# Performance work log

Measured on AMD Instinct MI355X. Metric: run time of the kernel, lower is better.

Reference implementation:

```python
import jax, jax.numpy as jnp
import numpy as np
from jax.scipy.special import logsumexp

NUM_TAGS = 48
SEQ_LEN = 512
BATCH = 1024


def setup_inputs() -> dict:
    key = jax.random.key(0)
    k_em, k_tags, k_tr, k_st, k_en = jax.random.split(key, 5)
    emissions = jax.random.normal(k_em, (SEQ_LEN, BATCH, NUM_TAGS), dtype=jnp.float32)
    tags = jax.random.randint(k_tags, (SEQ_LEN, BATCH), 0, NUM_TAGS, dtype=jnp.int64)
    mask = jnp.ones((SEQ_LEN, BATCH), dtype=jnp.int32)
    # CRF parameters, uniform(-0.1, 0.1) like reset_parameters
    transitions = jax.random.uniform(k_tr, (NUM_TAGS, NUM_TAGS), jnp.float32, -0.1, 0.1)
    start_transitions = jax.random.uniform(k_st, (NUM_TAGS,), jnp.float32, -0.1, 0.1)
    end_transitions = jax.random.uniform(k_en, (NUM_TAGS,), jnp.float32, -0.1, 0.1)
    return {
        "emissions": emissions,
        "tags": tags,
        "mask": mask,
        "transitions": transitions,
        "start_transitions": start_transitions,
        "end_transitions": end_transitions,
    }


def _score(emissions, tags, mask, transitions, start_transitions, end_transitions):
    # emissions: (S,B,T)  tags/mask: (S,B)
    S, B = tags.shape
    batch_idx = jnp.arange(B)
    maskf = mask.astype(emissions.dtype)
    # emission score at the gold tag for every timestep: (S,B)
    em_sc = jnp.take_along_axis(emissions, tags[..., None], axis=2)[..., 0]
    score = start_transitions[tags[0]] + em_sc[0]
    # transition score for steps 1..S-1: (S-1,B)
    trans_sc = transitions[tags[:-1], tags[1:]]
    score = score + ((trans_sc + em_sc[1:]) * maskf[1:]).sum(axis=0)
    valid_last_idx = mask.astype(jnp.int32).sum(axis=0) - 1  # (B,)
    last_tags = tags[valid_last_idx, batch_idx]
    return score + end_transitions[last_tags]


def _partition(emissions, mask, transitions, start_transitions, end_transitions):
    alpha0 = start_transitions[None, :] + emissions[0]  # (B,T)

    def step(alpha, inp):
        em_i, m_i = inp  # (B,T), (B,)
        # (B,T_prev,1) + (T_prev,T_cur) + (B,1,T_cur) -> logsumexp over prev
        cur = logsumexp(alpha[:, :, None] + transitions[None, :, :] + em_i[:, None, :], axis=1)
        alpha = jnp.where(m_i.astype(bool)[:, None], cur, alpha)
        return alpha, None

    alpha, _ = jax.lax.scan(step, alpha0, (emissions[1:], mask[1:]))
    return logsumexp(alpha + end_transitions[None, :], axis=1)  # (B,)


def reference(emissions, tags, mask, transitions, start_transitions, end_transitions):
    score = _score(emissions, tags, mask, transitions, start_transitions, end_transitions)
    partition = _partition(emissions, mask, transitions, start_transitions, end_transitions)
    nllh = partition - score
    return nllh.sum()  # reduction='sum'
```

## Files before the change

### kernel.cpp

```cpp
#include <hip/hip_runtime.h>

#define S 512
#define B 1024
#define K 48
#define LN2 0.6931471805599453f
#define PF 8

__global__ void __launch_bounds__(64) zero_out(float* o) {
    if (threadIdx.x == 0) o[0] = 0.f;
}

__device__ __forceinline__ float matvec48(const float4* f, const float* eT) {
    float s0 = 0.f, s1 = 0.f, s2 = 0.f, s3 = 0.f;
    #pragma unroll
    for (int i = 0; i < 12; ++i) {
        s0 = fmaf(f[i].x, eT[4 * i + 0], s0);
        s1 = fmaf(f[i].y, eT[4 * i + 1], s1);
        s2 = fmaf(f[i].z, eT[4 * i + 2], s2);
        s3 = fmaf(f[i].w, eT[4 * i + 3], s3);
    }
    return (s0 + s1) + (s2 + s3);
}

__global__ void __launch_bounds__(64) crf_kernel(
    const float* __restrict__ em, const int* __restrict__ tags,
    const int* __restrict__ mask, const float* __restrict__ trans,
    const float* __restrict__ start_tr, const float* __restrict__ end_tr,
    float* __restrict__ out)
{
    const int b    = blockIdx.x;
    const int lane = threadIdx.x;
    __shared__ __align__(16) float sh[K];

    float sc = 0.f;
    int mcnt = 0;
    #pragma unroll
    for (int i = 0; i < S / 64; ++i) {
        int t   = lane + 64 * i;
        int tag = tags[t * B + b];
        int mk  = mask[t * B + b];
        mcnt += mk;
        if (t == 0) {
            sc += start_tr[tag] + em[(size_t)b * K + tag];
        } else {
            int tagp  = tags[(t - 1) * B + b];
            float add = trans[tagp * K + tag] + em[((size_t)t * B + b) * K + tag];
            sc += mk ? add : 0.f;
        }
    }
    #pragma unroll
    for (int off = 32; off > 0; off >>= 1) {
        sc   += __shfl_xor(sc, off);
        mcnt += __shfl_xor(mcnt, off);
    }
    int last_t = mcnt - 1;
    if (last_t < 0) last_t += S;
    sc += end_tr[tags[last_t * B + b]];

    const int  j      = (lane < K) ? lane : 0;
    const bool active = lane < K;

    float eT[K];
    #pragma unroll
    for (int k = 0; k < K; ++k)
        eT[k] = __expf(trans[k * K + j]);

    float a      = __expf(start_tr[j] + em[(size_t)b * K + j]);
    int   offset = 0;
    float scale  = 1.0f;

    if (active) sh[j] = a;
    const float4* shv = (const float4*)sh;
    float4 f[12];
    #pragma unroll
    for (int i = 0; i < 12; ++i) f[i] = shv[i];

    float em_raw[PF];
    int   mk_n[PF];
    #pragma unroll
    for (int i = 0; i < PF; ++i) {
        em_raw[i] = em[((size_t)(1 + i) * B + b) * K + j];
        mk_n[i]   = mask[(size_t)(1 + i) * B + b];
    }
    float eexp_cur = __expf(em_raw[0]);

#define STEP(u_, t_, PFON_)                                                     \
    do {                                                                        \
        float s_   = matvec48(f, eT);                                           \
        float an_  = s_ * eexp_cur;                                             \
        a = mk_n[u_] ? an_ : a;                       \
        a *= scale;                          \
        if (lane < K) sh[lane] = a;                                             \
        _Pragma("unroll")                                                       \
        for (int i2_ = 0; i2_ < 12; ++i2_) f[i2_] = shv[i2_];                   \
        eexp_cur = __expf(em_raw[((u_) + 1) & 7]);           \
        if (PFON_) {                                                            \
            int tp_ = (t_) + PF;                                                \
            if (tp_ < S) {                                                      \
                em_raw[u_] = em[((size_t)tp_ * B + b) * K + j];                 \
                mk_n[u_]   = mask[(size_t)tp_ * B + b];                         \
            }                                                                   \
        }                                                                       \
        if (((u_) & 3) == 3) {               \
            int bits_ = __builtin_amdgcn_readlane(__float_as_int(a), 0);        \
            int E_    = ((bits_ >> 23) & 255) - 127;                            \
            offset += E_;                                                       \
            scale = __int_as_float((127 - E_) << 23);                           \
        } else {                                                                \
            scale = 1.0f;                                                       \
        }                                                                       \
    } while (0)

    for (int t0 = 1; t0 <= S - 2 * PF + 1; t0 += PF) {
        #pragma unroll
        for (int u = 0; u < PF; ++u) {
            STEP(u, t0 + u, true);
        }
    }
    #pragma unroll
    for (int u = 0; u < PF - 1; ++u) {
        STEP(u, (S - PF + 1) + u, false);
    }
#undef STEP

    float val = active ? a * __expf(end_tr[j]) : 0.f;
    #pragma unroll
    for (int off = 32; off > 0; off >>= 1) val += __shfl_xor(val, off);
    float partition = (float)offset * LN2 + __logf(val);

    if (lane == 0) atomicAdd(out, partition - sc);
}

extern "C" void kernel_launch(void* const* d_in, const int* in_sizes, int n_in,
                              void* d_out, int out_size, void* d_ws, size_t ws_size,
                              hipStream_t stream) {
    const float* em       = (const float*)d_in[0];
    const int*   tags     = (const int*)d_in[1];
    const int*   mask     = (const int*)d_in[2];
    const float* trans    = (const float*)d_in[3];
    const float* start_tr = (const float*)d_in[4];
    const float* end_tr   = (const float*)d_in[5];
    float* out = (float*)d_out;

    zero_out<<<dim3(1), dim3(64), 0, stream>>>(out);
    crf_kernel<<<dim3(B), dim3(64), 0, stream>>>(em, tags, mask, trans,
                                                 start_tr, end_tr, out);
}
```

Measured before the change: 319.4 us.

## Process two batch rows per wavefront to interleave independent recurrences

```diff
diff --git a/kernel.cpp b/kernel.cpp
--- a/kernel.cpp
+++ b/kernel.cpp
@@ -5,6 +5,7 @@
 #define K 48
 #define LN2 0.6931471805599453f
 #define PF 8
+#define NBLK 512
 
 __global__ void __launch_bounds__(64) zero_out(float* o) {
     if (threadIdx.x == 0) o[0] = 0.f;
@@ -28,107 +29,131 @@
     const float* __restrict__ start_tr, const float* __restrict__ end_tr,
     float* __restrict__ out)
 {
-    const int b    = blockIdx.x;
     const int lane = threadIdx.x;
-    __shared__ __align__(16) float sh[K];
+    const int b0   = blockIdx.x;
+    const int b1   = blockIdx.x + NBLK;
+    __shared__ __align__(16) float sh[2][K];
 
-    float sc = 0.f;
-    int mcnt = 0;
+    float scA = 0.f, scB = 0.f;
+    int mcA = 0, mcB = 0;
     #pragma unroll
     for (int i = 0; i < S / 64; ++i) {
-        int t   = lane + 64 * i;
-        int tag = tags[t * B + b];
-        int mk  = mask[t * B + b];
-        mcnt += mk;
-        if (t == 0) {
-            sc += start_tr[tag] + em[(size_t)b * K + tag];
-        } else {
-            int tagp  = tags[(t - 1) * B + b];
-            float add = trans[tagp * K + tag] + em[((size_t)t * B + b) * K + tag];
-            sc += mk ? add : 0.f;
+        int t = lane + 64 * i;
+        {
+            int tag = tags[t * B + b0];
+            int mk  = mask[t * B + b0];
+            mcA += mk;
+            if (t == 0) scA += start_tr[tag] + em[(size_t)b0 * K + tag];
+            else {
+                int tagp = tags[(t - 1) * B + b0];
+                float add = trans[tagp * K + tag] + em[((size_t)t * B + b0) * K + tag];
+                scA += mk ? add : 0.f;
+            }
+        }
+        {
+            int tag = tags[t * B + b1];
+            int mk  = mask[t * B + b1];
+            mcB += mk;
+            if (t == 0) scB += start_tr[tag] + em[(size_t)b1 * K + tag];
+            else {
+                int tagp = tags[(t - 1) * B + b1];
+                float add = trans[tagp * K + tag] + em[((size_t)t * B + b1) * K + tag];
+                scB += mk ? add : 0.f;
+            }
         }
     }
     #pragma unroll
     for (int off = 32; off > 0; off >>= 1) {
-        sc   += __shfl_xor(sc, off);
-        mcnt += __shfl_xor(mcnt, off);
+        scA += __shfl_xor(scA, off);
+        scB += __shfl_xor(scB, off);
+        mcA += __shfl_xor(mcA, off);
+        mcB += __shfl_xor(mcB, off);
     }
-    int last_t = mcnt - 1;
-    if (last_t < 0) last_t += S;
-    sc += end_tr[tags[last_t * B + b]];
+    int lA = mcA - 1; if (lA < 0) lA += S;
+    int lB = mcB - 1; if (lB < 0) lB += S;
+    scA += end_tr[tags[lA * B + b0]];
+    scB += end_tr[tags[lB * B + b1]];
 
     const int  j      = (lane < K) ? lane : 0;
     const bool active = lane < K;
 
     float eT[K];
     #pragma unroll
-    for (int k = 0; k < K; ++k)
-        eT[k] = __expf(trans[k * K + j]);
+    for (int k = 0; k < K; ++k) eT[k] = __expf(trans[k * K + j]);
 
-    float a      = __expf(start_tr[j] + em[(size_t)b * K + j]);
-    int   offset = 0;
-    float scale  = 1.0f;
+    float aA = __expf(start_tr[j] + em[(size_t)b0 * K + j]);
+    float aB = __expf(start_tr[j] + em[(size_t)b1 * K + j]);
+    int   offA = 0, offB = 0;
+    float sclA = 1.f, sclB = 1.f;
 
-    if (active) sh[j] = a;
-    const float4* shv = (const float4*)sh;
-    float4 f[12];
-    #pragma unroll
-    for (int i = 0; i < 12; ++i) f[i] = shv[i];
+    if (active) { sh[0][j] = aA; sh[1][j] = aB; }
+    const float4* shA = (const float4*)sh[0];
+    const float4* shB = (const float4*)sh[1];
 
-    float em_raw[PF];
-    int   mk_n[PF];
+    float emA[PF], emB[PF];
+    int   mkA[PF], mkB[PF];
     #pragma unroll
     for (int i = 0; i < PF; ++i) {
-        em_raw[i] = em[((size_t)(1 + i) * B + b) * K + j];
-        mk_n[i]   = mask[(size_t)(1 + i) * B + b];
+        emA[i] = em[((size_t)(1 + i) * B + b0) * K + j];
+        emB[i] = em[((size_t)(1 + i) * B + b1) * K + j];
+        mkA[i] = mask[(size_t)(1 + i) * B + b0];
+        mkB[i] = mask[(size_t)(1 + i) * B + b1];
     }
-    float eexp_cur = __expf(em_raw[0]);
+    float eexpA = __expf(emA[0]);
+    float eexpB = __expf(emB[0]);
 
-#define STEP(u_, t_, PFON_)                                                     \
+#define STEP2(u_, t_, PFON_)                                                    \
     do {                                                                        \
-        float s_   = matvec48(f, eT);                                           \
-        float an_  = s_ * eexp_cur;                                             \
-        a = mk_n[u_] ? an_ : a;                       \
-        a *= scale;                          \
-        if (lane < K) sh[lane] = a;                                             \
-        _Pragma("unroll")                                                       \
-        for (int i2_ = 0; i2_ < 12; ++i2_) f[i2_] = shv[i2_];                   \
-        eexp_cur = __expf(em_raw[((u_) + 1) & 7]);           \
+        float4 fA_[12], fB_[12];                                                \
+        _Pragma("unroll") for (int i_ = 0; i_ < 12; ++i_) fA_[i_] = shA[i_];    \
+        _Pragma("unroll") for (int i_ = 0; i_ < 12; ++i_) fB_[i_] = shB[i_];    \
+        float sA_ = matvec48(fA_, eT);                                          \
+        float sB_ = matvec48(fB_, eT);                                          \
+        float anA_ = sA_ * eexpA;                                               \
+        float anB_ = sB_ * eexpB;                                               \
+        aA = mkA[u_] ? anA_ : aA;  aA *= sclA;                                  \
+        aB = mkB[u_] ? anB_ : aB;  aB *= sclB;                                  \
+        if (lane < K) { sh[0][lane] = aA; sh[1][lane] = aB; }                   \
+        eexpA = __expf(emA[((u_) + 1) & 7]);                                    \
+        eexpB = __expf(emB[((u_) + 1) & 7]);                                    \
         if (PFON_) {                                                            \
             int tp_ = (t_) + PF;                                                \
             if (tp_ < S) {                                                      \
-                em_raw[u_] = em[((size_t)tp_ * B + b) * K + j];                 \
-                mk_n[u_]   = mask[(size_t)tp_ * B + b];                         \
+                emA[u_] = em[((size_t)tp_ * B + b0) * K + j];                   \
+                emB[u_] = em[((size_t)tp_ * B + b1) * K + j];                   \
+                mkA[u_] = mask[(size_t)tp_ * B + b0];                           \
+                mkB[u_] = mask[(size_t)tp_ * B + b1];                           \
             }                                                                   \
         }                                                                       \
-        if (((u_) & 3) == 3) {               \
-            int bits_ = __builtin_amdgcn_readlane(__float_as_int(a), 0);        \
-            int E_    = ((bits_ >> 23) & 255) - 127;                            \
-            offset += E_;                                                       \
-            scale = __int_as_float((127 - E_) << 23);                           \
-        } else {                                                                \
-            scale = 1.0f;                                                       \
-        }                                                                       \
+        if (((u_) & 7) == 7) {      \
+            int bA_ = __builtin_amdgcn_readlane(__float_as_int(aA), 0);         \
+            int bB_ = __builtin_amdgcn_readlane(__float_as_int(aB), 0);         \
+            int EA_ = ((bA_ >> 23) & 255) - 127;                                \
+            int EB_ = ((bB_ >> 23) & 255) - 127;                                \
+            offA += EA_;  sclA = __int_as_float((127 - EA_) << 23);             \
+            offB += EB_;  sclB = __int_as_float((127 - EB_) << 23);             \
+        } else { sclA = 1.f; sclB = 1.f; }                                      \
     } while (0)
 
     for (int t0 = 1; t0 <= S - 2 * PF + 1; t0 += PF) {
         #pragma unroll
-        for (int u = 0; u < PF; ++u) {
-            STEP(u, t0 + u, true);
-        }
+        for (int u = 0; u < PF; ++u) STEP2(u, t0 + u, true);
     }
     #pragma unroll
-    for (int u = 0; u < PF - 1; ++u) {
-        STEP(u, (S - PF + 1) + u, false);
+    for (int u = 0; u < PF - 1; ++u) STEP2(u, (S - PF + 1) + u, false);
+#undef STEP2
+
+    float vA = active ? aA * __expf(end_tr[j]) : 0.f;
+    float vB = active ? aB * __expf(end_tr[j]) : 0.f;
+    #pragma unroll
+    for (int off = 32; off > 0; off >>= 1) {
+        vA += __shfl_xor(vA, off);
+        vB += __shfl_xor(vB, off);
     }
-#undef STEP
+    float pA = (float)offA * LN2 + __logf(vA);
+    float pB = (float)offB * LN2 + __logf(vB);
 
-    float val = active ? a * __expf(end_tr[j]) : 0.f;
-    #pragma unroll
-    for (int off = 32; off > 0; off >>= 1) val += __shfl_xor(val, off);
-    float partition = (float)offset * LN2 + __logf(val);
-
-    if (lane == 0) atomicAdd(out, partition - sc);
+    if (lane == 0) atomicAdd(out, (pA - scA) + (pB - scB));
 }
 
 extern "C" void kernel_launch(void* const* d_in, const int* in_sizes, int n_in,
@@ -143,6 +168,6 @@
     float* out = (float*)d_out;
 
     zero_out<<<dim3(1), dim3(64), 0, stream>>>(out);
-    crf_kernel<<<dim3(B), dim3(64), 0, stream>>>(em, tags, mask, trans,
-                                                 start_tr, end_tr, out);
+    crf_kernel<<<dim3(NBLK), dim3(64), 0, stream>>>(em, tags, mask, trans,
+                                                    start_tr, end_tr, out);
 }
```

Result: slower. 422.0 us (+32.1%).
